# Performance work log

Hardware: AMD Instinct MI355X
Metric: run time of the kernel (lower is better)

Reference implementation:

```python
import jax, jax.numpy as jnp
import numpy as np

B, S, D, H, HD = 1, 2048, 1024, 16, 64
WINDOW = 512
RADIUS = max(1, WINDOW // 2)
GLOBAL_IDX = (0, 1, 2, 3)
NEG = -1e9


def rotate_half(x):
    x1, x2 = jnp.split(x, 2, axis=-1)
    return jnp.concatenate([-x2, x1], axis=-1)


def apply_rope(x, cos, sin, pos):
    # x: [b, s, h, hd]; cos/sin: [max_pos, hd]; pos: [b, s]
    c = cos[pos][:, :, None, :]
    s_ = sin[pos][:, :, None, :]
    return x * c + rotate_half(x) * s_


def setup_inputs() -> dict:
    key = jax.random.key(0)
    ks = jax.random.split(key, 12)
    x = jax.random.normal(ks[0], (B, S, D), dtype=jnp.float32)
    # RoPE tables (standard construction)
    inv_freq = 1.0 / (10000.0 ** (jnp.arange(0, HD, 2, dtype=jnp.float32) / HD))
    t = jnp.arange(S, dtype=jnp.float32)
    freqs = jnp.outer(t, inv_freq)                      # [S, HD/2]
    emb = jnp.concatenate([freqs, freqs], axis=-1)      # [S, HD]
    cos_freqs = jnp.cos(emb)
    sin_freqs = jnp.sin(emb)
    position_ids = jnp.broadcast_to(jnp.arange(S, dtype=jnp.int32), (B, S))
    w = lambda k: jax.random.normal(k, (D, D), dtype=jnp.float32) * 0.02
    return {
        "x": x, "cos_freqs": cos_freqs, "sin_freqs": sin_freqs,
        "position_ids": position_ids,
        "Wqs": w(ks[1]), "Wks": w(ks[2]), "Wvs": w(ks[3]),
        "Wqg": w(ks[4]), "Wkg": w(ks[5]), "Wvg": w(ks[6]),
        "Wo": w(ks[7]),
    }


def reference(x, cos_freqs, sin_freqs, position_ids, Wqs, Wks, Wvs, Wqg, Wkg, Wvg, Wo):
    b, s, d = x.shape
    split = lambda y: y.reshape(b, s, H, HD)
    qs = split(x @ Wqs)
    ks_ = split(x @ Wks)
    vs = split(x @ Wvs)
    kg = split(x @ Wkg)
    vg = split(x @ Wvg)
    # (qg projection exists in the module but is unused by its forward math)
    qs = apply_rope(qs, cos_freqs, sin_freqs, position_ids)
    ks_ = apply_rope(ks_, cos_freqs, sin_freqs, position_ids)

    qs_t = jnp.swapaxes(qs, 1, 2)   # [b,h,s,hd]
    ks_t = jnp.swapaxes(ks_, 1, 2)
    vs_t = jnp.swapaxes(vs, 1, 2)
    scale = 1.0 / jnp.sqrt(jnp.float32(HD))

    # local sliding-window (causal) attention over dense scores
    scores = jnp.einsum('bhsd,bhtd->bhst', qs_t, ks_t) * scale
    i = jnp.arange(s)[:, None]
    j = jnp.arange(s)[None, :]
    mask = (jnp.abs(i - j) <= RADIUS) & (j <= i)
    scores = jnp.where(mask[None, None], scores, NEG)
    g = jnp.array(GLOBAL_IDX)
    scores = scores.at[:, :, :, g].add(1e9)  # same as per-index set(score+1e9)
    attn = jax.nn.softmax(scores, axis=-1)
    out_local = jnp.einsum('bhst,bhtd->bhsd', attn, vs_t)
    out_local = jnp.swapaxes(out_local, 1, 2).reshape(b, s, d)

    # global attention: all queries attend to the global-index columns of kg/vg
    kg_t = jnp.swapaxes(kg, 1, 2)
    vg_t = jnp.swapaxes(vg, 1, 2)
    scores_g = jnp.einsum('bhsd,bhtd->bhst', qs_t, kg_t) * scale
    col_mask = jnp.zeros((s,), dtype=bool).at[g].set(True)
    scores_g = jnp.where(col_mask[None, None, None, :], scores_g, NEG)
    attn_g = jax.nn.softmax(scores_g, axis=-1)
    out_global = jnp.einsum('bhst,bhtd->bhsd', attn_g, vg_t)
    out_global = jnp.swapaxes(out_global, 1, 2).reshape(b, s, d)

    return (out_local + out_global) @ Wo
```

## Files before the change

kernel.cpp:

```cpp
#include <hip/hip_runtime.h>

typedef _Float16 half8 __attribute__((ext_vector_type(8)));
typedef float floatx4 __attribute__((ext_vector_type(4)));

#define SEQ 2048
#define DMODEL 1024
#define NHEADS 16
#define HEADDIM 64
#define PW 5120

__global__ __launch_bounds__(256) void k_prep(
    const float* __restrict__ x,
    const float* __restrict__ w0, const float* __restrict__ w1, const float* __restrict__ w2,
    const float* __restrict__ w3, const float* __restrict__ w4, const float* __restrict__ w5,
    _Float16* __restrict__ xh, _Float16* __restrict__ wcat, _Float16* __restrict__ wot) {
  const int tid = threadIdx.x;
  const int b = blockIdx.x;
  if (b < 1024) {
    int base = b * 2048 + tid * 8;
    floatx4 f0 = *(const floatx4*)(x + base);
    floatx4 f1 = *(const floatx4*)(x + base + 4);
    half8 h;
    #pragma unroll
    for (int e = 0; e < 4; ++e) { h[e] = (_Float16)f0[e]; h[e + 4] = (_Float16)f1[e]; }
    *(half8*)(xh + base) = h;
    return;
  }
  __shared__ _Float16 T[64][72];
  int t = b - 1024;
  int z = t >> 8;
  int tile = t & 255;
  int k0 = (tile >> 4) * 64, n0 = (tile & 15) * 64;
  const float* W = (z == 0) ? w0 : (z == 1) ? w1 : (z == 2) ? w2
                 : (z == 3) ? w3 : (z == 4) ? w4 : w5;
  _Float16* dst = (z < 5) ? (wcat + (size_t)z * 1024 * 1024) : wot;

  int lr = tid >> 2, c0 = (tid & 3) * 16;
  #pragma unroll
  for (int i = 0; i < 4; ++i) {
    floatx4 f = *(const floatx4*)(W + (size_t)(k0 + lr) * DMODEL + n0 + c0 + i * 4);
    #pragma unroll
    for (int e = 0; e < 4; ++e) T[c0 + i * 4 + e][lr] = (_Float16)f[e];
  }
  __syncthreads();
  int nr = tid >> 2, s0 = (tid & 3) * 16;
  #pragma unroll
  for (int i = 0; i < 2; ++i) {
    half8 h = *(const half8*)&T[nr][s0 + i * 8];
    *(half8*)(dst + (size_t)(n0 + nr) * DMODEL + k0 + s0 + i * 8) = h;
  }
}

template <bool HALF_OUT, bool FUSE_ROPE, bool SPARSE>
__global__ __launch_bounds__(256, 2) void k_gemm128b(
    const _Float16* __restrict__ A, const _Float16* __restrict__ Bt,
    void* __restrict__ Cv, float* __restrict__ Cp0, float* __restrict__ Cp1,
    const float* __restrict__ cos_t, const float* __restrict__ sin_t,
    const int* __restrict__ pos, int M, int N, int K, int kLen) {
  __shared__ _Float16 As[128][128];
  __shared__ _Float16 Bs[128][128];
  const int tid = threadIdx.x;
  const int lane = tid & 63;
  const int w = tid >> 6;
  const int wm = (w >> 1) * 64;
  const int wn = (w & 1) * 64;
  const int l15 = lane & 15;
  const int q4 = lane >> 4;
  int m0, n0, kStart;
  if (SPARSE) {
    int b = blockIdx.x;
    if (b < 384) { m0 = (b & 15) * 128; n0 = (b >> 4) * 128; }
    else         { m0 = 0;              n0 = 3072 + (b - 384) * 128; }
    kStart = 0;
  } else {
    m0 = blockIdx.x * 128;
    n0 = blockIdx.y * 128;
    kStart = blockIdx.z * kLen;
  }

  floatx4 acc[4][4];
  #pragma unroll
  for (int i = 0; i < 4; ++i)
    #pragma unroll
    for (int j = 0; j < 4; ++j) acc[i][j] = (floatx4){0.f, 0.f, 0.f, 0.f};

  _Float16* asBase = &As[0][0];
  _Float16* bsBase = &Bs[0][0];
  const int swz = l15 & 7;

  for (int k0 = kStart; k0 < kStart + kLen; k0 += 128) {
    __syncthreads();
    #pragma unroll
    for (int it = 0; it < 8; ++it) {
      int c = it * 256 + tid;
      int r = c >> 4, cc = c & 15;
      int g = cc ^ (r & 7);
      __builtin_amdgcn_global_load_lds(
          (const __attribute__((address_space(1))) void*)(A + (size_t)(m0 + r) * K + k0 + g * 8),
          (__attribute__((address_space(3))) void*)(asBase + (it * 256 + w * 64) * 8),
          16, 0, 0);
      __builtin_amdgcn_global_load_lds(
          (const __attribute__((address_space(1))) void*)(Bt + (size_t)(n0 + r) * K + k0 + g * 8),
          (__attribute__((address_space(3))) void*)(bsBase + (it * 256 + w * 64) * 8),
          16, 0, 0);
    }
    __syncthreads();

    #pragma unroll
    for (int kk = 0; kk < 4; ++kk) {
      int q = kk * 4 + q4;
      half8 af[4], bf[4];
      #pragma unroll
      for (int t = 0; t < 4; ++t) {
        int ar = wm + t * 16 + l15;
        af[t] = *(const half8*)(asBase + (size_t)ar * 128 + ((q ^ swz) * 8));
        int br = wn + t * 16 + l15;
        bf[t] = *(const half8*)(bsBase + (size_t)br * 128 + ((q ^ swz) * 8));
      }
      #pragma unroll
      for (int i = 0; i < 4; ++i)
        #pragma unroll
        for (int j = 0; j < 4; ++j)
          acc[i][j] = __builtin_amdgcn_mfma_f32_16x16x32_f16(af[i], bf[j], acc[i][j], 0, 0, 0);
    }
  }

  float* P = HALF_OUT ? nullptr : ((!SPARSE && blockIdx.z) ? Cp1 : Cp0);
  #pragma unroll
  for (int tm = 0; tm < 4; ++tm) {
    #pragma unroll
    for (int r = 0; r < 4; ++r) {
      int row = m0 + wm + tm * 16 + q4 * 4 + r;
      float v[4];
      #pragma unroll
      for (int tn = 0; tn < 4; ++tn) v[tn] = acc[tm][tn][r];
      if (FUSE_ROPE && n0 < 2048) {
        int p = pos[row];
        #pragma unroll
        for (int tn = 0; tn < 2; ++tn) {
          int d = tn * 16 + l15;
          float a = acc[tm][tn][r];
          float bvv = acc[tm][tn + 2][r];
          float c1 = cos_t[p * 64 + d],      s1 = sin_t[p * 64 + d];
          float c2 = cos_t[p * 64 + d + 32], s2 = sin_t[p * 64 + d + 32];
          v[tn]     = a * c1 - bvv * s1;
          v[tn + 2] = bvv * c2 + a * s2;
        }
      }
      #pragma unroll
      for (int tn = 0; tn < 4; ++tn) {
        int col = n0 + wn + tn * 16 + l15;
        if (HALF_OUT)
          ((_Float16*)Cv)[(size_t)row * N + col] = (_Float16)v[tn];
        else
          P[(size_t)row * N + col] = v[tn];
      }
    }
  }
}

__global__ __launch_bounds__(256) void k_reduce(const float* __restrict__ p0,
                                                const float* __restrict__ p1,
                                                float* __restrict__ out) {
  int i = (blockIdx.x * 256 + threadIdx.x) * 4;
  floatx4 a = *(const floatx4*)(p0 + i);
  floatx4 b = *(const floatx4*)(p1 + i);
  *(floatx4*)(out + i) = a + b;
}

__global__ __launch_bounds__(256, 2) void k_attn(const _Float16* __restrict__ proj,
                                                 _Float16* __restrict__ out) {
  const int tid = threadIdx.x;
  const int hb = blockIdx.y * 64;

  if (blockIdx.x >= 14) {
    const int i = (blockIdx.x - 14) * 4 + (tid >> 6);
    const int lane = tid & 63;
    const float scale = 0.125f;
    float qv = (float)proj[(size_t)i * PW + hb + lane];
    float sg[4];
    #pragma unroll
    for (int g = 0; g < 4; ++g) {
      float kgv = (float)proj[(size_t)g * PW + 3072 + hb + lane];
      float v = qv * kgv;
      #pragma unroll
      for (int off = 32; off; off >>= 1) v += __shfl_xor(v, off, 64);
      sg[g] = v * scale;
    }
    float mg = fmaxf(fmaxf(sg[0], sg[1]), fmaxf(sg[2], sg[3]));
    float dg = 0.f, og = 0.f;
    #pragma unroll
    for (int g = 0; g < 4; ++g) {
      float p = __expf(sg[g] - mg);
      dg += p;
      og += p * (float)proj[(size_t)g * PW + 4096 + hb + lane];
    }
    og /= dg;
    int jmin = (i >= 256) ? (i - 256) : 0;
    int jmax = (i < 3) ? i : 3;
    float acc = 0.f;
    for (int j = jmin; j <= jmax; ++j)
      acc += (float)proj[(size_t)j * PW + 2048 + hb + lane];
    float ol = acc / (float)(jmax - jmin + 1);
    out[(size_t)i * DMODEL + hb + lane] = (_Float16)(ol + og);
    return;
  }

  const int i0 = 256 + blockIdx.x * 128;
  const int jlo = i0 - 256;
  const int lane = tid & 63;
  const int w = tid >> 6;
  const int l15 = lane & 15;
  const int q4 = lane >> 4;

  __shared__ _Float16 Qs[128][72];
  __shared__ _Float16 Kc[64][72];
  __shared__ _Float16 Vtc[64][72];
  __shared__ _Float16 Ps[128][72];
  __shared__ _Float16 kg_s[4][64];
  __shared__ _Float16 vg_s[4][64];
  __shared__ float svg_s[64];
  __shared__ float pg_s[4][128];

  #pragma unroll
  for (int rep = 0; rep < 4; ++rep) {
    int c = tid + rep * 256;
    int r = c >> 3, q = c & 7;
    *(half8*)&Qs[r][q * 8] = *(const half8*)(proj + (size_t)(i0 + r) * PW + hb + q * 8);
  }
  {
    int g = tid >> 6, c2 = tid & 63;
    kg_s[g][c2] = proj[(size_t)g * PW + 3072 + hb + c2];
    vg_s[g][c2] = proj[(size_t)g * PW + 4096 + hb + c2];
    if (tid < 64) {
      float s = 0.f;
      #pragma unroll
      for (int g2 = 0; g2 < 4; ++g2) s += (float)proj[(size_t)g2 * PW + 2048 + hb + tid];
      svg_s[tid] = s;
    }
  }
  __syncthreads();

  #pragma unroll
  for (int pass = 0; pass < 2; ++pass) {
    int ro = pass * 64 + w * 16 + (lane >> 2);
    int part = lane & 3;
    float sg[4];
    #pragma unroll
    for (int g = 0; g < 4; ++g) {
      float acc = 0.f;
      #pragma unroll
      for (int u = 0; u < 16; ++u)
        acc += (float)Qs[ro][part * 16 + u] * (float)kg_s[g][part * 16 + u];
      acc += __shfl_xor(acc, 1, 64);
      acc += __shfl_xor(acc, 2, 64);
      sg[g] = acc * 0.125f;
    }
    float mg = fmaxf(fmaxf(sg[0], sg[1]), fmaxf(sg[2], sg[3]));
    float dg = 0.f;
    #pragma unroll
    for (int g = 0; g < 4; ++g) dg += __expf(sg[g] - mg);
    pg_s[part][ro] = __expf(sg[part] - mg) / dg;
  }

  half8 qf[2][2];
  #pragma unroll
  for (int rg = 0; rg < 2; ++rg) {
    int row = w * 32 + rg * 16 + l15;
    qf[rg][0] = *(const half8*)&Qs[row][q4 * 8];
    qf[rg][1] = *(const half8*)&Qs[row][32 + q4 * 8];
  }

  float m_r[2][4], l_r[2][4];
  floatx4 oacc[2][4];
  #pragma unroll
  for (int rg = 0; rg < 2; ++rg)
    #pragma unroll
    for (int cb = 0; cb < 4; ++cb) {
      oacc[rg][cb] = (floatx4){0.f, 0.f, 0.f, 0.f};
      m_r[rg][cb] = 0.f;
      l_r[rg][cb] = 4.f;
    }

  for (int cc = 0; cc < 6; ++cc) {
    const int jbase = jlo + cc * 64;
    __syncthreads();
    #pragma unroll
    for (int rep = 0; rep < 2; ++rep) {
      int c = tid + rep * 256;
      int r = c >> 3, q = c & 7;
      *(half8*)&Kc[r][q * 8] =
          *(const half8*)(proj + (size_t)(jbase + r) * PW + 1024 + hb + q * 8);
    }
    #pragma unroll
    for (int it = 0; it < 2; ++it) {
      int idx = it * 256 + tid;
      int j = (idx & 7) + ((idx >> 6) << 3);
      int d0 = ((idx >> 3) & 7) * 8;
      half8 vv = *(const half8*)(proj + (size_t)(jbase + j) * PW + 2048 + hb + d0);
      #pragma unroll
      for (int u = 0; u < 8; ++u) Vtc[d0 + u][j] = vv[u];
    }
    __syncthreads();

    #pragma unroll
    for (int rg = 0; rg < 2; ++rg) {
      float sc[4][4];
      #pragma unroll
      for (int cb = 0; cb < 4; ++cb) {
        half8 b0 = *(const half8*)&Kc[cb * 16 + l15][q4 * 8];
        half8 b1 = *(const half8*)&Kc[cb * 16 + l15][32 + q4 * 8];
        floatx4 a = (floatx4){0.f, 0.f, 0.f, 0.f};
        a = __builtin_amdgcn_mfma_f32_16x16x32_f16(qf[rg][0], b0, a, 0, 0, 0);
        a = __builtin_amdgcn_mfma_f32_16x16x32_f16(qf[rg][1], b1, a, 0, 0, 0);
        #pragma unroll
        for (int r = 0; r < 4; ++r) sc[cb][r] = a[r];
      }

      #pragma unroll
      for (int r = 0; r < 4; ++r) {
        int ri = w * 32 + rg * 16 + q4 * 4 + r;
        float rowmax = -1e30f;
        #pragma unroll
        for (int cb = 0; cb < 4; ++cb) {
          int jjg = cc * 64 + cb * 16 + l15;
          bool valid = (jjg >= ri) && (jjg <= ri + 256);
          float s = valid ? sc[cb][r] * 0.125f : -1e30f;
          sc[cb][r] = s;
          rowmax = fmaxf(rowmax, s);
        }
        #pragma unroll
        for (int off = 1; off < 16; off <<= 1)
          rowmax = fmaxf(rowmax, __shfl_xor(rowmax, off, 64));
        float m_new = fmaxf(m_r[rg][r], rowmax);
        float alpha = __expf(m_r[rg][r] - m_new);
        float rs = 0.f;
        #pragma unroll
        for (int cb = 0; cb < 4; ++cb) {
          float p = __expf(sc[cb][r] - m_new);
          Ps[ri][cb * 16 + l15] = (_Float16)p;
          rs += p;
        }
        #pragma unroll
        for (int off = 1; off < 16; off <<= 1) rs += __shfl_xor(rs, off, 64);
        l_r[rg][r] = l_r[rg][r] * alpha + rs;
        m_r[rg][r] = m_new;
        #pragma unroll
        for (int cb = 0; cb < 4; ++cb) oacc[rg][cb][r] *= alpha;
      }

      half8 pf0 = *(const half8*)&Ps[w * 32 + rg * 16 + l15][q4 * 8];
      half8 pf1 = *(const half8*)&Ps[w * 32 + rg * 16 + l15][32 + q4 * 8];
      #pragma unroll
      for (int cb = 0; cb < 4; ++cb) {
        half8 v0 = *(const half8*)&Vtc[cb * 16 + l15][q4 * 8];
        half8 v1 = *(const half8*)&Vtc[cb * 16 + l15][32 + q4 * 8];
        oacc[rg][cb] = __builtin_amdgcn_mfma_f32_16x16x32_f16(pf0, v0, oacc[rg][cb], 0, 0, 0);
        oacc[rg][cb] = __builtin_amdgcn_mfma_f32_16x16x32_f16(pf1, v1, oacc[rg][cb], 0, 0, 0);
      }
    }
  }

  #pragma unroll
  for (int rg = 0; rg < 2; ++rg)
    #pragma unroll
    for (int r = 0; r < 4; ++r) {
      int ri = w * 32 + rg * 16 + q4 * 4 + r;
      if (i0 + ri < 260) continue;
      float e0 = __expf(-m_r[rg][r]);
      float inv = 1.f / l_r[rg][r];
      #pragma unroll
      for (int cb = 0; cb < 4; ++cb) {
        int col = cb * 16 + l15;
        float ol = (oacc[rg][cb][r] + e0 * svg_s[col]) * inv;
        float og = 0.f;
        #pragma unroll
        for (int g = 0; g < 4; ++g) og += pg_s[g][ri] * (float)vg_s[g][col];
        out[(size_t)(i0 + ri) * DMODEL + hb + col] = (_Float16)(ol + og);
      }
    }
}

extern "C" void kernel_launch(void* const* d_in, const int* in_sizes, int n_in,
                              void* d_out, int out_size, void* d_ws, size_t ws_size,
                              hipStream_t stream) {
  const float* x     = (const float*)d_in[0];
  const float* cos_t = (const float*)d_in[1];
  const float* sin_t = (const float*)d_in[2];
  const int*   pos   = (const int*)d_in[3];
  const float* Wqs   = (const float*)d_in[4];
  const float* Wks   = (const float*)d_in[5];
  const float* Wvs   = (const float*)d_in[6];
  const float* Wkg   = (const float*)d_in[8];
  const float* Wvg   = (const float*)d_in[9];
  const float* Wo    = (const float*)d_in[10];
  float* out = (float*)d_out;

  char* ws = (char*)d_ws;
  _Float16* xh   = (_Float16*)(ws);
  _Float16* wcat = (_Float16*)(ws + (4u << 20));
  _Float16* wot  = (_Float16*)(ws + (14u << 20));
  _Float16* proj = (_Float16*)(ws + (16u << 20));
  _Float16* attn = (_Float16*)(ws + (36u << 20));
  float* p0 = (float*)(ws);
  float* p1 = (float*)(ws + (16u << 20));

  k_prep<<<2560, 256, 0, stream>>>(x, Wqs, Wks, Wvs, Wkg, Wvg, Wo, xh, wcat, wot);
  k_gemm128b<true, true, true><<<400, 256, 0, stream>>>(
      xh, wcat, proj, nullptr, nullptr, cos_t, sin_t, pos, SEQ, PW, DMODEL, DMODEL);
  k_attn<<<dim3(79, NHEADS), 256, 0, stream>>>(proj, attn);
  k_gemm128b<false, false, false><<<dim3(16, 8, 2), 256, 0, stream>>>(
      attn, wot, nullptr, p0, p1, cos_t, sin_t, pos, SEQ, DMODEL, DMODEL, 512);
  k_reduce<<<SEQ * DMODEL / 1024, 256, 0, stream>>>(p0, p1, out);
}
```

Baseline: 172.0 us.

## Drop split-K output GEMM and widen attention key chunks to 128

The output projection GEMM no longer splits K across two blocks. It writes fp32 results straight to the output, which removes the partial buffers and the separate reduce kernel launch. The attention kernel now processes keys in 3 chunks of 128 instead of 6 chunks of 64, which halves the barriers and online-softmax rescales. It also reads Q fragments directly from global memory instead of staging them in LDS. The trade-off is half as many blocks for the output GEMM (128 vs 256), which lowers parallelism, plus larger LDS tiles and more registers in attention.

```diff
diff --git a/kernel.cpp b/kernel.cpp
--- a/kernel.cpp
+++ b/kernel.cpp
@@ -54,7 +54,7 @@
 template <bool HALF_OUT, bool FUSE_ROPE, bool SPARSE>
 __global__ __launch_bounds__(256, 2) void k_gemm128b(
     const _Float16* __restrict__ A, const _Float16* __restrict__ Bt,
-    void* __restrict__ Cv, float* __restrict__ Cp0, float* __restrict__ Cp1,
+    void* __restrict__ Cv, float* __restrict__ Cp0,
     const float* __restrict__ cos_t, const float* __restrict__ sin_t,
     const int* __restrict__ pos, int M, int N, int K, int kLen) {
   __shared__ _Float16 As[128][128];
@@ -66,16 +66,14 @@
   const int wn = (w & 1) * 64;
   const int l15 = lane & 15;
   const int q4 = lane >> 4;
-  int m0, n0, kStart;
+  int m0, n0;
   if (SPARSE) {
     int b = blockIdx.x;
     if (b < 384) { m0 = (b & 15) * 128; n0 = (b >> 4) * 128; }
     else         { m0 = 0;              n0 = 3072 + (b - 384) * 128; }
-    kStart = 0;
   } else {
     m0 = blockIdx.x * 128;
     n0 = blockIdx.y * 128;
-    kStart = blockIdx.z * kLen;
   }
 
   floatx4 acc[4][4];
@@ -88,7 +86,7 @@
   _Float16* bsBase = &Bs[0][0];
   const int swz = l15 & 7;
 
-  for (int k0 = kStart; k0 < kStart + kLen; k0 += 128) {
+  for (int k0 = 0; k0 < kLen; k0 += 128) {
     __syncthreads();
     #pragma unroll
     for (int it = 0; it < 8; ++it) {
@@ -125,7 +123,6 @@
     }
   }
 
-  float* P = HALF_OUT ? nullptr : ((!SPARSE && blockIdx.z) ? Cp1 : Cp0);
   #pragma unroll
   for (int tm = 0; tm < 4; ++tm) {
     #pragma unroll
@@ -153,19 +150,10 @@
         if (HALF_OUT)
           ((_Float16*)Cv)[(size_t)row * N + col] = (_Float16)v[tn];
         else
-          P[(size_t)row * N + col] = v[tn];
-      }
-    }
-  }
-}
-
-__global__ __launch_bounds__(256) void k_reduce(const float* __restrict__ p0,
-                                                const float* __restrict__ p1,
-                                                float* __restrict__ out) {
-  int i = (blockIdx.x * 256 + threadIdx.x) * 4;
-  floatx4 a = *(const floatx4*)(p0 + i);
-  floatx4 b = *(const floatx4*)(p1 + i);
-  *(floatx4*)(out + i) = a + b;
+          Cp0[(size_t)row * N + col] = v[tn];
+      }
+    }
+  }
 }
 
 __global__ __launch_bounds__(256, 2) void k_attn(const _Float16* __restrict__ proj,
@@ -213,21 +201,14 @@
   const int l15 = lane & 15;
   const int q4 = lane >> 4;
 
-  __shared__ _Float16 Qs[128][72];
-  __shared__ _Float16 Kc[64][72];
-  __shared__ _Float16 Vtc[64][72];
-  __shared__ _Float16 Ps[128][72];
+  __shared__ _Float16 Kc[128][72];
+  __shared__ _Float16 Vtc[64][136];
+  __shared__ _Float16 Ps[128][136];
   __shared__ _Float16 kg_s[4][64];
   __shared__ _Float16 vg_s[4][64];
   __shared__ float svg_s[64];
   __shared__ float pg_s[4][128];
 
-  #pragma unroll
-  for (int rep = 0; rep < 4; ++rep) {
-    int c = tid + rep * 256;
-    int r = c >> 3, q = c & 7;
-    *(half8*)&Qs[r][q * 8] = *(const half8*)(proj + (size_t)(i0 + r) * PW + hb + q * 8);
-  }
   {
     int g = tid >> 6, c2 = tid & 63;
     kg_s[g][c2] = proj[(size_t)g * PW + 3072 + hb + c2];
@@ -245,13 +226,14 @@
   for (int pass = 0; pass < 2; ++pass) {
     int ro = pass * 64 + w * 16 + (lane >> 2);
     int part = lane & 3;
+    const _Float16* qrow = proj + (size_t)(i0 + ro) * PW + hb + part * 16;
     float sg[4];
     #pragma unroll
     for (int g = 0; g < 4; ++g) {
       float acc = 0.f;
       #pragma unroll
       for (int u = 0; u < 16; ++u)
-        acc += (float)Qs[ro][part * 16 + u] * (float)kg_s[g][part * 16 + u];
+        acc += (float)qrow[u] * (float)kg_s[g][part * 16 + u];
       acc += __shfl_xor(acc, 1, 64);
       acc += __shfl_xor(acc, 2, 64);
       sg[g] = acc * 0.125f;
@@ -266,9 +248,9 @@
   half8 qf[2][2];
   #pragma unroll
   for (int rg = 0; rg < 2; ++rg) {
-    int row = w * 32 + rg * 16 + l15;
-    qf[rg][0] = *(const half8*)&Qs[row][q4 * 8];
-    qf[rg][1] = *(const half8*)&Qs[row][32 + q4 * 8];
+    const _Float16* qp = proj + (size_t)(i0 + w * 32 + rg * 16 + l15) * PW + hb;
+    qf[rg][0] = *(const half8*)(qp + q4 * 8);
+    qf[rg][1] = *(const half8*)(qp + 32 + q4 * 8);
   }
 
   float m_r[2][4], l_r[2][4];
@@ -282,32 +264,31 @@
       l_r[rg][cb] = 4.f;
     }
 
-  for (int cc = 0; cc < 6; ++cc) {
-    const int jbase = jlo + cc * 64;
+  for (int cc = 0; cc < 3; ++cc) {
+    const int jbase = jlo + cc * 128;
     __syncthreads();
     #pragma unroll
-    for (int rep = 0; rep < 2; ++rep) {
-      int c = tid + rep * 256;
+    for (int it = 0; it < 4; ++it) {
+      int c = it * 256 + tid;
       int r = c >> 3, q = c & 7;
       *(half8*)&Kc[r][q * 8] =
           *(const half8*)(proj + (size_t)(jbase + r) * PW + 1024 + hb + q * 8);
     }
     #pragma unroll
-    for (int it = 0; it < 2; ++it) {
-      int idx = it * 256 + tid;
-      int j = (idx & 7) + ((idx >> 6) << 3);
-      int d0 = ((idx >> 3) & 7) * 8;
-      half8 vv = *(const half8*)(proj + (size_t)(jbase + j) * PW + 2048 + hb + d0);
-      #pragma unroll
-      for (int u = 0; u < 8; ++u) Vtc[d0 + u][j] = vv[u];
+    for (int it = 0; it < 4; ++it) {
+      int u = it * 256 + tid;
+      int j = u >> 3, o = u & 7;
+      half8 vv = *(const half8*)(proj + (size_t)(jbase + j) * PW + 2048 + hb + o * 8);
+      #pragma unroll
+      for (int e = 0; e < 8; ++e) Vtc[o * 8 + e][j] = vv[e];
     }
     __syncthreads();
 
     #pragma unroll
     for (int rg = 0; rg < 2; ++rg) {
-      float sc[4][4];
-      #pragma unroll
-      for (int cb = 0; cb < 4; ++cb) {
+      float sc[8][4];
+      #pragma unroll
+      for (int cb = 0; cb < 8; ++cb) {
         half8 b0 = *(const half8*)&Kc[cb * 16 + l15][q4 * 8];
         half8 b1 = *(const half8*)&Kc[cb * 16 + l15][32 + q4 * 8];
         floatx4 a = (floatx4){0.f, 0.f, 0.f, 0.f};
@@ -322,8 +303,8 @@
         int ri = w * 32 + rg * 16 + q4 * 4 + r;
         float rowmax = -1e30f;
         #pragma unroll
-        for (int cb = 0; cb < 4; ++cb) {
-          int jjg = cc * 64 + cb * 16 + l15;
+        for (int cb = 0; cb < 8; ++cb) {
+          int jjg = cc * 128 + cb * 16 + l15;
           bool valid = (jjg >= ri) && (jjg <= ri + 256);
           float s = valid ? sc[cb][r] * 0.125f : -1e30f;
           sc[cb][r] = s;
@@ -336,7 +317,7 @@
         float alpha = __expf(m_r[rg][r] - m_new);
         float rs = 0.f;
         #pragma unroll
-        for (int cb = 0; cb < 4; ++cb) {
+        for (int cb = 0; cb < 8; ++cb) {
           float p = __expf(sc[cb][r] - m_new);
           Ps[ri][cb * 16 + l15] = (_Float16)p;
           rs += p;
@@ -349,14 +330,18 @@
         for (int cb = 0; cb < 4; ++cb) oacc[rg][cb][r] *= alpha;
       }
 
-      half8 pf0 = *(const half8*)&Ps[w * 32 + rg * 16 + l15][q4 * 8];
-      half8 pf1 = *(const half8*)&Ps[w * 32 + rg * 16 + l15][32 + q4 * 8];
+      half8 pf[4];
+      int prow = w * 32 + rg * 16 + l15;
+      #pragma unroll
+      for (int kb = 0; kb < 4; ++kb)
+        pf[kb] = *(const half8*)&Ps[prow][kb * 32 + q4 * 8];
       #pragma unroll
       for (int cb = 0; cb < 4; ++cb) {
-        half8 v0 = *(const half8*)&Vtc[cb * 16 + l15][q4 * 8];
-        half8 v1 = *(const half8*)&Vtc[cb * 16 + l15][32 + q4 * 8];
-        oacc[rg][cb] = __builtin_amdgcn_mfma_f32_16x16x32_f16(pf0, v0, oacc[rg][cb], 0, 0, 0);
-        oacc[rg][cb] = __builtin_amdgcn_mfma_f32_16x16x32_f16(pf1, v1, oacc[rg][cb], 0, 0, 0);
+        #pragma unroll
+        for (int kb = 0; kb < 4; ++kb) {
+          half8 vf = *(const half8*)&Vtc[cb * 16 + l15][(kb * 4 + q4) * 8];
+          oacc[rg][cb] = __builtin_amdgcn_mfma_f32_16x16x32_f16(pf[kb], vf, oacc[rg][cb], 0, 0, 0);
+        }
       }
     }
   }
@@ -402,14 +387,11 @@
   _Float16* wot  = (_Float16*)(ws + (14u << 20));
   _Float16* proj = (_Float16*)(ws + (16u << 20));
   _Float16* attn = (_Float16*)(ws + (36u << 20));
-  float* p0 = (float*)(ws);
-  float* p1 = (float*)(ws + (16u << 20));
 
   k_prep<<<2560, 256, 0, stream>>>(x, Wqs, Wks, Wvs, Wkg, Wvg, Wo, xh, wcat, wot);
   k_gemm128b<true, true, true><<<400, 256, 0, stream>>>(
-      xh, wcat, proj, nullptr, nullptr, cos_t, sin_t, pos, SEQ, PW, DMODEL, DMODEL);
+      xh, wcat, proj, nullptr, cos_t, sin_t, pos, SEQ, PW, DMODEL, DMODEL);
   k_attn<<<dim3(79, NHEADS), 256, 0, stream>>>(proj, attn);
-  k_gemm128b<false, false, false><<<dim3(16, 8, 2), 256, 0, stream>>>(
-      attn, wot, nullptr, p0, p1, cos_t, sin_t, pos, SEQ, DMODEL, DMODEL, 512);
-  k_reduce<<<SEQ * DMODEL / 1024, 256, 0, stream>>>(p0, p1, out);
+  k_gemm128b<false, false, false><<<dim3(16, 8), 256, 0, stream>>>(
+      attn, wot, nullptr, out, cos_t, sin_t, pos, SEQ, DMODEL, DMODEL, DMODEL);
 }
```

Measured after the change: 187.3 us. 8.9% more time.

## Drop Q shared staging, pad transposed V tile, raise attention occupancy

Applied to the files above, without the earlier changes.

The attention kernel no longer stages Q in shared memory. The global-score pass and the MFMA Q fragments now read Q straight from global memory. The transposed V tile gets an extra 8-element offset every 8 rows to reduce bank conflicts on the transposing stores, and launch bounds move from 2 to 4 blocks per SM. Less shared memory and the higher occupancy target aim to hide latency better, but the compiler may be forced to limit registers, and the Q reads become uncoalesced global loads.

```diff
diff --git a/kernel.cpp b/kernel.cpp
--- a/kernel.cpp
+++ b/kernel.cpp
@@ -168,7 +168,7 @@
   *(floatx4*)(out + i) = a + b;
 }
 
-__global__ __launch_bounds__(256, 2) void k_attn(const _Float16* __restrict__ proj,
+__global__ __launch_bounds__(256, 4) void k_attn(const _Float16* __restrict__ proj,
                                                  _Float16* __restrict__ out) {
   const int tid = threadIdx.x;
   const int hb = blockIdx.y * 64;
@@ -213,21 +213,15 @@
   const int l15 = lane & 15;
   const int q4 = lane >> 4;
 
-  __shared__ _Float16 Qs[128][72];
   __shared__ _Float16 Kc[64][72];
-  __shared__ _Float16 Vtc[64][72];
+  __shared__ _Float16 VtcB[64 * 72 + 64];
   __shared__ _Float16 Ps[128][72];
   __shared__ _Float16 kg_s[4][64];
   __shared__ _Float16 vg_s[4][64];
   __shared__ float svg_s[64];
   __shared__ float pg_s[4][128];
-
-  #pragma unroll
-  for (int rep = 0; rep < 4; ++rep) {
-    int c = tid + rep * 256;
-    int r = c >> 3, q = c & 7;
-    *(half8*)&Qs[r][q * 8] = *(const half8*)(proj + (size_t)(i0 + r) * PW + hb + q * 8);
-  }
+  #define VTI(d, j) ((d) * 72 + ((d) >> 3) * 8 + (j))
+
   {
     int g = tid >> 6, c2 = tid & 63;
     kg_s[g][c2] = proj[(size_t)g * PW + 3072 + hb + c2];
@@ -245,13 +239,14 @@
   for (int pass = 0; pass < 2; ++pass) {
     int ro = pass * 64 + w * 16 + (lane >> 2);
     int part = lane & 3;
+    const _Float16* qrow = proj + (size_t)(i0 + ro) * PW + hb + part * 16;
     float sg[4];
     #pragma unroll
     for (int g = 0; g < 4; ++g) {
       float acc = 0.f;
       #pragma unroll
       for (int u = 0; u < 16; ++u)
-        acc += (float)Qs[ro][part * 16 + u] * (float)kg_s[g][part * 16 + u];
+        acc += (float)qrow[u] * (float)kg_s[g][part * 16 + u];
       acc += __shfl_xor(acc, 1, 64);
       acc += __shfl_xor(acc, 2, 64);
       sg[g] = acc * 0.125f;
@@ -266,9 +261,9 @@
   half8 qf[2][2];
   #pragma unroll
   for (int rg = 0; rg < 2; ++rg) {
-    int row = w * 32 + rg * 16 + l15;
-    qf[rg][0] = *(const half8*)&Qs[row][q4 * 8];
-    qf[rg][1] = *(const half8*)&Qs[row][32 + q4 * 8];
+    const _Float16* qp = proj + (size_t)(i0 + w * 32 + rg * 16 + l15) * PW + hb;
+    qf[rg][0] = *(const half8*)(qp + q4 * 8);
+    qf[rg][1] = *(const half8*)(qp + 32 + q4 * 8);
   }
 
   float m_r[2][4], l_r[2][4];
@@ -299,7 +294,7 @@
       int d0 = ((idx >> 3) & 7) * 8;
       half8 vv = *(const half8*)(proj + (size_t)(jbase + j) * PW + 2048 + hb + d0);
       #pragma unroll
-      for (int u = 0; u < 8; ++u) Vtc[d0 + u][j] = vv[u];
+      for (int e = 0; e < 8; ++e) VtcB[VTI(d0 + e, j)] = vv[e];
     }
     __syncthreads();
 
@@ -349,12 +344,14 @@
         for (int cb = 0; cb < 4; ++cb) oacc[rg][cb][r] *= alpha;
       }
 
-      half8 pf0 = *(const half8*)&Ps[w * 32 + rg * 16 + l15][q4 * 8];
-      half8 pf1 = *(const half8*)&Ps[w * 32 + rg * 16 + l15][32 + q4 * 8];
+      int prow = w * 32 + rg * 16 + l15;
+      half8 pf0 = *(const half8*)&Ps[prow][q4 * 8];
+      half8 pf1 = *(const half8*)&Ps[prow][32 + q4 * 8];
       #pragma unroll
       for (int cb = 0; cb < 4; ++cb) {
-        half8 v0 = *(const half8*)&Vtc[cb * 16 + l15][q4 * 8];
-        half8 v1 = *(const half8*)&Vtc[cb * 16 + l15][32 + q4 * 8];
+        int vd = cb * 16 + l15;
+        half8 v0 = *(const half8*)&VtcB[VTI(vd, 0) + q4 * 8];
+        half8 v1 = *(const half8*)&VtcB[VTI(vd, 0) + 32 + q4 * 8];
         oacc[rg][cb] = __builtin_amdgcn_mfma_f32_16x16x32_f16(pf0, v0, oacc[rg][cb], 0, 0, 0);
         oacc[rg][cb] = __builtin_amdgcn_mfma_f32_16x16x32_f16(pf1, v1, oacc[rg][cb], 0, 0, 0);
       }
```

New measurement: 196.5 us. 1.14x slower.
